# Performance work log

Measured on AMD Instinct MI355X. Metric: run time of the kernel, lower is better.

Reference implementation:

```python
import jax, jax.numpy as jnp
import numpy as np


def _conv(x, w):
    # SpykeTorch snn.Convolution: plain conv2d, no bias, no padding (VALID)
    return jax.lax.conv_general_dilated(
        x, w, window_strides=(1, 1), padding='VALID',
        dimension_numbers=('NCHW', 'OIHW', 'NCHW'))


def _pad2(x, p=2):
    # sf.pad(input, pad=(2,2,2,2), value=0): zero-pad last two (spatial) dims
    return jnp.pad(x, ((0, 0), (0, 0), (p, p), (p, p)))


def _fire(pot, thr):
    # sf.fire: thresholded[pot <= thr] = 0 ; spk = thresholded.sign()
    thresholded = jnp.where(pot > thr, pot, jnp.zeros((), pot.dtype))
    spk = (pot > thr).astype(pot.dtype)
    return spk, thresholded


def _pool(x, k, s):
    # sf.pooling: max_pool2d, floor mode (== VALID reduce_window)
    return jax.lax.reduce_window(
        x, -jnp.inf, jax.lax.max,
        window_dimensions=(1, 1, k, k),
        window_strides=(1, 1, s, s),
        padding='VALID')


def setup_inputs() -> dict:
    key = jax.random.key(0)
    kx, k1, k2, k3 = jax.random.split(key, 4)
    # (T, C, H, W): T timesteps act as batch in SpykeTorch
    x = jax.random.uniform(kx, (20, 6, 160, 160), dtype=jnp.float32)

    def xavier_normal(k, shape):
        fan_in = shape[1] * shape[2] * shape[3]
        fan_out = shape[0] * shape[2] * shape[3]
        std = float(np.sqrt(2.0 / (fan_in + fan_out)))
        return jax.random.normal(k, shape, dtype=jnp.float32) * std

    w1 = xavier_normal(k1, (30, 6, 4, 4))
    w2 = xavier_normal(k2, (250, 30, 3, 3))
    w3 = xavier_normal(k3, (200, 250, 3, 3))
    return {'x': x, 'w1': w1, 'w2': w2, 'w3': w3, 'layer_idx': 3}


def reference(x, w1, w2, w3, layer_idx):
    # Eval-mode forward path of deepSNN up to `layer_idx` (tensor-returning branches)
    CONV1_T, CONV2_T, CONV3_T = 1.0, 1.0, 25.0
    inp = _pad2(x.astype(jnp.float32))          # (T,6,164,164)
    pot = _conv(inp, w1)                        # (T,30,161,161)
    spk, pot = _fire(pot, CONV1_T)
    if layer_idx == 1:
        return spk, pot
    pot = _conv(_pad2(_pool(spk, 2, 2)), w2)    # (T,250,82,82)
    spk, pot = _fire(pot, CONV2_T)
    if layer_idx == 2:
        return spk, pot
    pot = _conv(_pad2(_pool(spk, 3, 3)), w3)    # (T,200,29,29)
    spk, pot = _fire(pot, CONV3_T)
    return spk, pot
```

## Files before the change

kernel.cpp:

```cpp
#include <hip/hip_runtime.h>


#define OUT_HALF 3364000
#define MASK_PLANE 128000
#define T_FLOATS 168200

typedef float v2f __attribute__((ext_vector_type(2)));

__global__ __launch_bounds__(256, 4) void k_conv1(const float* __restrict__ x,
                                                  const float* __restrict__ w1,
                                                  const float* __restrict__ w2,
                                                  float* __restrict__ w2t,
                                                  unsigned int* __restrict__ mask1,
                                                  unsigned int* __restrict__ flags2) {
    if (blockIdx.x >= 1500) {
        int tb = blockIdx.x - 1500;
        int tid = threadIdx.x;
        if (tb == 0)
            for (int i = tid; i < 540; i += 256) flags2[i] = 0u;
        int idx = tb * 256 + tid;
        if (idx < 67500) {
            int oc = idx / 270, ck = idx % 270;
            w2t[ck * 250 + oc] = w2[idx];
        }
        return;
    }

    __shared__ float in_lds[6 * 35 * 40];

    int b = blockIdx.x;
    int h = b % 3;     b /= 3;
    int colt = b % 5;  b /= 5;
    int rowt = b % 5;  b /= 5;
    int t = b;
    int ph0 = rowt * 16, pw0 = colt * 16;
    int i0 = 2 * ph0, j0 = 2 * pw0;
    int tid = threadIdx.x;

    for (int idx = tid; idx < 2100; idx += 256) {
        int v4 = idx % 10;
        int row = idx / 10;
        int c = row / 35, rr = row % 35;
        int gr = i0 + rr - 2;
        int gc0 = j0 - 4 + 4 * v4;
        float4 v; v.x = 0.f; v.y = 0.f; v.z = 0.f; v.w = 0.f;
        if ((unsigned)gr < 160u && (unsigned)gc0 < 160u)
            v = *(const float4*)&x[((t * 6 + c) * 160 + gr) * 160 + gc0];
        float* dst = &in_lds[row * 40];
        int m = 2 * v4;
        dst[m]      = v.x;
        dst[m + 20] = v.y;
        dst[m + 1]  = v.z;
        dst[m + 21] = v.w;
    }
    __syncthreads();

    int pw_l = tid & 15, ph_l = tid >> 4;
    int rb = 2 * ph_l;

    v2f acc01[10], acc23[10];
#pragma unroll
    for (int o = 0; o < 10; ++o) {
        acc01[o] = (v2f)(0.f);
        acc23[o] = (v2f)(0.f);
    }

    const float4* wq = (const float4*)w1 + h * 10 * 24;

#pragma unroll 1
    for (int c = 0; c < 6; ++c) {
        const float* pl = &in_lds[(c * 35 + rb) * 40 + pw_l];
        float q[5][5];
#pragma unroll
        for (int r = 0; r < 5; ++r) {
            const float* pr = pl + r * 40;
            q[r][0] = pr[1];  q[r][1] = pr[21]; q[r][2] = pr[2];
            q[r][3] = pr[22]; q[r][4] = pr[3];
        }
        v2f p[5][4];
#pragma unroll
        for (int r = 0; r < 5; ++r)
#pragma unroll
            for (int k = 0; k < 4; ++k) {
                p[r][k].x = q[r][k];
                p[r][k].y = q[r][k + 1];
            }
#pragma unroll
        for (int o = 0; o < 10; ++o) {
            const float4* wp = wq + o * 24 + c * 4;
#pragma unroll
            for (int kh = 0; kh < 4; ++kh) {
                float4 wv = wp[kh];
                v2f w0 = {wv.x, wv.x}, w1v = {wv.y, wv.y};
                v2f w2v = {wv.z, wv.z}, w3v = {wv.w, wv.w};
                acc01[o] += p[kh][0] * w0;   acc23[o] += p[kh + 1][0] * w0;
                acc01[o] += p[kh][1] * w1v;  acc23[o] += p[kh + 1][1] * w1v;
                acc01[o] += p[kh][2] * w2v;  acc23[o] += p[kh + 1][2] * w2v;
                acc01[o] += p[kh][3] * w3v;  acc23[o] += p[kh + 1][3] * w3v;
            }
        }
    }

    unsigned int msk = 0;
#pragma unroll
    for (int o = 0; o < 10; ++o) {
        bool s = acc01[o].x > 1.f || acc01[o].y > 1.f ||
                 acc23[o].x > 1.f || acc23[o].y > 1.f;
        if (s) msk |= 1u << o;
    }
    mask1[h * MASK_PLANE + (t * 80 + ph0 + ph_l) * 80 + pw0 + pw_l] = msk;
}

__global__ __launch_bounds__(256) void k_conv2(const unsigned int* __restrict__ mask1,
                                               const float* __restrict__ w2t,
                                               unsigned long long* __restrict__ pool2m,
                                               unsigned int* __restrict__ flags2) {
    __shared__ unsigned int m_lds[5 * 84];
    __shared__ int f2;

    int b = blockIdx.x;
    int ninth = b % 9;  b /= 9;
    int ph = b % 27;
    int t = b / 27;
    int tid = threadIdx.x;
    int ocl = tid & 63, wv = tid >> 6;
    int r0 = 3 * ph - 2;
    int pwA = ninth * 3;

    if (tid == 0) f2 = 0;
    for (int idx = tid; idx < 420; idx += 256) {
        int r = idx / 84, col = idx % 84;
        int gr = r0 + r, gc = col - 2;
        unsigned int v = 0;
        if ((unsigned)gr < 80u && (unsigned)gc < 80u) {
            int i2 = (t * 80 + gr) * 80 + gc;
            v = mask1[i2] | (mask1[MASK_PLANE + i2] << 10) |
                (mask1[2 * MASK_PLANE + i2] << 20);
        }
        m_lds[idx] = v;
    }
    __syncthreads();

    int oc = wv * 64 + ocl;
    const float* wb = w2t + oc;
    bool valid = oc < 250;
    unsigned long long* prow = pool2m + ((t * 27 + ph) * 27) * 4 + wv;

    {
        int c0A = 3 * pwA, c0B = c0A + 3;
        unsigned int qA[25], qB[25];
#pragma unroll
        for (int dr = 0; dr < 5; ++dr)
#pragma unroll
            for (int ds = 0; ds < 5; ++ds) {
                qA[dr * 5 + ds] = m_lds[dr * 84 + c0A + ds];
                qB[dr * 5 + ds] = m_lds[dr * 84 + c0B + ds];
            }

        float accA[3][3], accB[3][3];
#pragma unroll
        for (int i = 0; i < 3; ++i)
#pragma unroll
            for (int j = 0; j < 3; ++j) { accA[i][j] = 0.f; accB[i][j] = 0.f; }

#pragma unroll
        for (int dr = 0; dr < 5; ++dr) {
#pragma unroll
            for (int ds = 0; ds < 5; ++ds) {
                unsigned int mA = qA[dr * 5 + ds];
                unsigned int mB = qB[dr * 5 + ds];
                while (mA | mB) {
                    bool hA = mA != 0, hB = mB != 0;
                    int cA = __builtin_ctz(mA | 0x40000000u);
                    int cB = __builtin_ctz(mB | 0x40000000u);
                    mA &= mA - 1;
                    mB &= mB - 1;
                    const float* pA = wb + cA * 2250;
                    const float* pB = wb + cB * 2250;
                    float vA[3][3], vB[3][3];
#pragma unroll
                    for (int i = 0; i < 3; ++i) {
                        if (dr - i < 0 || dr - i > 2) continue;
#pragma unroll
                        for (int j = 0; j < 3; ++j) {
                            if (ds - j < 0 || ds - j > 2) continue;
                            int off = ((dr - i) * 3 + (ds - j)) * 250;
                            vA[i][j] = pA[off];
                            vB[i][j] = pB[off];
                        }
                    }
#pragma unroll
                    for (int i = 0; i < 3; ++i) {
                        if (dr - i < 0 || dr - i > 2) continue;
#pragma unroll
                        for (int j = 0; j < 3; ++j) {
                            if (ds - j < 0 || ds - j > 2) continue;
                            accA[i][j] += hA ? vA[i][j] : 0.f;
                            accB[i][j] += hB ? vB[i][j] : 0.f;
                        }
                    }
                }
            }
        }

        bool sA = false, sB = false;
#pragma unroll
        for (int i = 0; i < 3; ++i)
#pragma unroll
            for (int j = 0; j < 3; ++j) {
                sA = sA || (accA[i][j] > 1.f);
                sB = sB || (accB[i][j] > 1.f);
            }
        unsigned long long bA = __ballot(sA && valid);
        unsigned long long bB = __ballot(sB && valid);
        if (ocl == 0) {
            prow[pwA * 4] = bA;
            prow[(pwA + 1) * 4] = bB;
        }
        if (bA | bB) f2 = 1;
    }

    {
        int pw = pwA + 2;
        int c0 = 3 * pw;
        unsigned int q[25];
#pragma unroll
        for (int dr = 0; dr < 5; ++dr)
#pragma unroll
            for (int ds = 0; ds < 5; ++ds)
                q[dr * 5 + ds] = m_lds[dr * 84 + c0 + ds];

        float acc[3][3];
#pragma unroll
        for (int i = 0; i < 3; ++i)
#pragma unroll
            for (int j = 0; j < 3; ++j) acc[i][j] = 0.f;

#pragma unroll
        for (int dr = 0; dr < 5; ++dr) {
#pragma unroll
            for (int ds = 0; ds < 5; ++ds) {
                unsigned int m = q[dr * 5 + ds];
                while (m) {
                    int c1 = __builtin_ctz(m); m &= m - 1;
                    bool has2 = (m != 0);
                    int c2 = c1;
                    if (has2) { c2 = __builtin_ctz(m); m &= m - 1; }
                    const float* p1 = wb + c1 * 2250;
                    const float* p2 = wb + c2 * 2250;
                    float v1[3][3], v2[3][3];
#pragma unroll
                    for (int i = 0; i < 3; ++i) {
                        if (dr - i < 0 || dr - i > 2) continue;
#pragma unroll
                        for (int j = 0; j < 3; ++j) {
                            if (ds - j < 0 || ds - j > 2) continue;
                            int off = ((dr - i) * 3 + (ds - j)) * 250;
                            v1[i][j] = p1[off];
                            v2[i][j] = p2[off];
                        }
                    }
#pragma unroll
                    for (int i = 0; i < 3; ++i) {
                        if (dr - i < 0 || dr - i > 2) continue;
#pragma unroll
                        for (int j = 0; j < 3; ++j) {
                            if (ds - j < 0 || ds - j > 2) continue;
                            acc[i][j] += v1[i][j];
                            acc[i][j] += has2 ? v2[i][j] : 0.f;
                        }
                    }
                }
            }
        }

        bool s = false;
#pragma unroll
        for (int i = 0; i < 3; ++i)
#pragma unroll
            for (int j = 0; j < 3; ++j) s = s || (acc[i][j] > 1.f);

        unsigned long long blt = __ballot(s && valid);
        if (ocl == 0) prow[pw * 4] = blt;
        if (blt) f2 = 1;
    }

    __syncthreads();
    if (tid == 0 && f2) flags2[t * 27 + ph] = 1u;
}

__global__ __launch_bounds__(320) void k_conv3(const unsigned long long* __restrict__ pool2m,
                                               const float* __restrict__ w3,
                                               float* __restrict__ out,
                                               const unsigned int* __restrict__ flags2) {
    __shared__ float w_lds[25 * 9 * 40];
    __shared__ float in_lds[25 * 4 * 34];

    int b = blockIdx.x;
    int rb = b % 15;  b /= 15;
    int ocg = b % 5;  b /= 5;
    int t = b;
    int oc0 = ocg * 40;
    int r0 = 2 * rb;
    int tid = threadIdx.x;
    int ocl = tid % 40, ct = tid / 40;

    {
        unsigned int fT = 0;
        const unsigned int* fp = flags2 + t * 27;
#pragma unroll
        for (int r = 0; r < 27; ++r) fT |= fp[r];
        if (fT == 0) {
            float4 z; z.x = 0.f; z.y = 0.f; z.z = 0.f; z.w = 0.f;
            float4* o0 = (float4*)(out + (size_t)t * T_FLOATS);
            float4* o1 = (float4*)(out + OUT_HALF + (size_t)t * T_FLOATS);
            int s = ocg * 15 + rb;
            int lo = s * 561;
            int hi = lo + 561; if (hi > 42050) hi = 42050;
            for (int i = lo + tid; i < hi; i += 320) {
                o0[i] = z;
                o1[i] = z;
            }
            return;
        }
    }

    {
        unsigned int f = 0;
        int rlo = r0 - 2; if (rlo < 0) rlo = 0;
        int rhi = r0 + 1; if (rhi > 26) rhi = 26;
        for (int r = rlo; r <= rhi; ++r) f |= flags2[t * 27 + r];
        if (f == 0) {
            int nrows = (r0 + 1 < 29) ? 2 : 1;
            int stride = 29 * nrows;
            int cnt = 40 * stride;
            for (int idx = tid; idx < cnt; idx += 320) {
                int o = idx / stride, rem = idx % stride;
                size_t base = (size_t)((t * 200 + oc0 + o) * 29 + r0) * 29 + rem;
                out[base] = 0.f;
                out[OUT_HALF + base] = 0.f;
            }
            return;
        }
    }

    float acc[2][4];
#pragma unroll
    for (int i = 0; i < 2; ++i)
#pragma unroll
        for (int j = 0; j < 4; ++j) acc[i][j] = 0.f;

    for (int chn = 0; chn < 10; ++chn) {
        int cc0 = chn * 25;
        for (int idx = tid; idx < 25 * 9 * 40; idx += 320) {
            int o = idx % 40, ck = idx / 40;
            int ckg = cc0 * 9 + ck;
            w_lds[idx] = w3[(size_t)(oc0 + o) * 2250 + ckg];
        }
        for (int idx = tid; idx < 25 * 4 * 34; idx += 320) {
            int col = idx % 34;
            int rem = idx / 34;
            int r = rem & 3, cl = rem >> 2;
            int gr = r0 + r - 2, gc = col - 2;
            float v = 0.f;
            if ((unsigned)gr < 27u && (unsigned)gc < 27u) {
                int c = cc0 + cl;
                unsigned long long wbits =
                    pool2m[((t * 27 + gr) * 27 + gc) * 4 + (c >> 6)];
                v = (float)((wbits >> (c & 63)) & 1ull);
            }
            in_lds[idx] = v;
        }
        __syncthreads();

        for (int cl = 0; cl < 25; ++cl) {
            float in[4][6];
#pragma unroll
            for (int r = 0; r < 4; ++r)
#pragma unroll
                for (int j = 0; j < 6; ++j)
                    in[r][j] = in_lds[(cl * 4 + r) * 34 + ct * 4 + j];
            const float* wp = &w_lds[cl * 360 + ocl];
#pragma unroll
            for (int k = 0; k < 9; ++k) {
                float w = wp[k * 40];
                int kh = k / 3, kw = k % 3;
#pragma unroll
                for (int i = 0; i < 2; ++i)
#pragma unroll
                    for (int j = 0; j < 4; ++j)
                        acc[i][j] += in[i + kh][j + kw] * w;
            }
        }
        __syncthreads();
    }

    {
        int oc = oc0 + ocl;
#pragma unroll
        for (int i = 0; i < 2; ++i) {
            int r = r0 + i;
            if (r < 29) {
#pragma unroll
                for (int j = 0; j < 4; ++j) {
                    int col = ct * 4 + j;
                    if (col < 29) {
                        float pot = acc[i][j];
                        bool s = pot > 25.f;
                        size_t base = ((size_t)((t * 200 + oc) * 29 + r)) * 29 + col;
                        out[base] = s ? 1.f : 0.f;
                        out[OUT_HALF + base] = s ? pot : 0.f;
                    }
                }
            }
        }
    }
}

extern "C" void kernel_launch(void* const* d_in, const int* in_sizes, int n_in,
                              void* d_out, int out_size, void* d_ws, size_t ws_size,
                              hipStream_t stream) {
    const float* x  = (const float*)d_in[0];
    const float* w1 = (const float*)d_in[1];
    const float* w2 = (const float*)d_in[2];
    const float* w3 = (const float*)d_in[3];
    float* out = (float*)d_out;

    unsigned int* mask1 = (unsigned int*)d_ws;
    unsigned long long* pool2m = (unsigned long long*)((char*)d_ws + 1536000);
    float* w2t = (float*)((char*)d_ws + 2002560);
    unsigned int* flags2 = (unsigned int*)((char*)d_ws + 2277376);

    k_conv1<<<1764, 256, 0, stream>>>(x, w1, w2, w2t, mask1, flags2);
    k_conv2<<<20 * 27 * 9, 256, 0, stream>>>(mask1, w2t, pool2m, flags2);
    k_conv3<<<20 * 5 * 15, 320, 0, stream>>>(pool2m, w3, out, flags2);
}
```

Before: 142.4 us.

## Compute conv1 with bf16 MFMA on a pre-padded input buffer

Replaces the scalar FP32 conv1 kernel with a new kernel that treats the 4x4x6 convolution as a small GEMM using 32x32x16 bf16 MFMA instructions. Pooled spike masks are built with wave ballots. A new prep kernel zero-pads the input into a workspace buffer and also absorbs the w2 transpose and flag clearing that conv1 used to do. The intent is to move conv1 arithmetic onto matrix cores. It costs an extra kernel launch, a full write and read of the padded input, and bf16 rounding that can flip spikes whose potential lies near the threshold.

```diff
diff --git a/kernel.cpp b/kernel.cpp
--- a/kernel.cpp
+++ b/kernel.cpp
@@ -1,21 +1,36 @@
 #include <hip/hip_runtime.h>
+#include <hip/hip_bf16.h>
 
 
 #define OUT_HALF 3364000
 #define MASK_PLANE 128000
 #define T_FLOATS 168200
 
-typedef float v2f __attribute__((ext_vector_type(2)));
-
-__global__ __launch_bounds__(256, 4) void k_conv1(const float* __restrict__ x,
-                                                  const float* __restrict__ w1,
-                                                  const float* __restrict__ w2,
-                                                  float* __restrict__ w2t,
-                                                  unsigned int* __restrict__ mask1,
-                                                  unsigned int* __restrict__ flags2) {
-    if (blockIdx.x >= 1500) {
-        int tb = blockIdx.x - 1500;
-        int tid = threadIdx.x;
+typedef float f32x16 __attribute__((ext_vector_type(16)));
+typedef short bf8s __attribute__((ext_vector_type(8)));
+typedef float f32x4 __attribute__((ext_vector_type(4)));
+typedef f32x4 f32x4u __attribute__((aligned(4)));
+
+static __device__ __forceinline__ unsigned int pkbf(float a, float b) {
+    union { __hip_bfloat162 h; unsigned int u; } cv;
+    cv.h = __float22bfloat162_rn(make_float2(a, b));
+    return cv.u;
+}
+static __device__ __forceinline__ unsigned short bfbits(float a) {
+    union { __hip_bfloat16 h; unsigned short u; } cv;
+    cv.h = __float2bfloat16(a);
+    return cv.u;
+}
+
+__global__ __launch_bounds__(256) void k_prep(const float* __restrict__ x,
+                                              const float* __restrict__ w2,
+                                              float* __restrict__ xpad,
+                                              float* __restrict__ w2t,
+                                              unsigned int* __restrict__ flags2) {
+    int bidx = blockIdx.x;
+    int tid = threadIdx.x;
+    if (bidx >= 1576) {
+        int tb = bidx - 1576;
         if (tb == 0)
             for (int i = tid; i < 540; i += 256) flags2[i] = 0u;
         int idx = tb * 256 + tid;
@@ -25,90 +40,85 @@
         }
         return;
     }
-
-    __shared__ float in_lds[6 * 35 * 40];
-
+    for (int e = bidx * 256 + tid; e < 3227520; e += 403456) {
+        int tc = e / 26896;
+        int rem = e - tc * 26896;
+        int r = rem / 164, col = rem - r * 164;
+        int sr = r - 2, sc = col - 2;
+        float v = 0.f;
+        if ((unsigned)sr < 160u && (unsigned)sc < 160u)
+            v = x[(tc * 160 + sr) * 160 + sc];
+        xpad[e] = v;
+    }
+}
+
+__global__ __launch_bounds__(256) void k_conv1m(const float* __restrict__ xpad,
+                                                const float* __restrict__ w1,
+                                                unsigned int* __restrict__ mask1) {
+    __shared__ unsigned short B_lds[6 * 64 * 8];
+
+    int tid = threadIdx.x;
+#pragma unroll
+    for (int n = 0; n < 12; ++n) {
+        int q = n * 256 + tid;
+        int i = q & 7, ll = (q >> 3) & 63, ks = q >> 9;
+        int oc = ll & 31;
+        int kg = ks * 16 + ((ll >> 5) << 3) + i;
+        float w = (oc < 30) ? w1[oc * 96 + kg] : 0.f;
+        B_lds[q] = bfbits(w);
+    }
+    __syncthreads();
+
+    int l = tid & 63, wv = tid >> 6;
     int b = blockIdx.x;
-    int h = b % 3;     b /= 3;
-    int colt = b % 5;  b /= 5;
-    int rowt = b % 5;  b /= 5;
-    int t = b;
-    int ph0 = rowt * 16, pw0 = colt * 16;
-    int i0 = 2 * ph0, j0 = 2 * pw0;
-    int tid = threadIdx.x;
-
-    for (int idx = tid; idx < 2100; idx += 256) {
-        int v4 = idx % 10;
-        int row = idx / 10;
-        int c = row / 35, rr = row % 35;
-        int gr = i0 + rr - 2;
-        int gc0 = j0 - 4 + 4 * v4;
-        float4 v; v.x = 0.f; v.y = 0.f; v.z = 0.f; v.w = 0.f;
-        if ((unsigned)gr < 160u && (unsigned)gc0 < 160u)
-            v = *(const float4*)&x[((t * 6 + c) * 160 + gr) * 160 + gc0];
-        float* dst = &in_lds[row * 40];
-        int m = 2 * v4;
-        dst[m]      = v.x;
-        dst[m + 20] = v.y;
-        dst[m + 1]  = v.z;
-        dst[m + 21] = v.w;
-    }
-    __syncthreads();
-
-    int pw_l = tid & 15, ph_l = tid >> 4;
-    int rb = 2 * ph_l;
-
-    v2f acc01[10], acc23[10];
-#pragma unroll
-    for (int o = 0; o < 10; ++o) {
-        acc01[o] = (v2f)(0.f);
-        acc23[o] = (v2f)(0.f);
-    }
-
-    const float4* wq = (const float4*)w1 + h * 10 * 24;
-
-#pragma unroll 1
-    for (int c = 0; c < 6; ++c) {
-        const float* pl = &in_lds[(c * 35 + rb) * 40 + pw_l];
-        float q[5][5];
-#pragma unroll
-        for (int r = 0; r < 5; ++r) {
-            const float* pr = pl + r * 40;
-            q[r][0] = pr[1];  q[r][1] = pr[21]; q[r][2] = pr[2];
-            q[r][3] = pr[22]; q[r][4] = pr[3];
-        }
-        v2f p[5][4];
-#pragma unroll
-        for (int r = 0; r < 5; ++r)
-#pragma unroll
-            for (int k = 0; k < 4; ++k) {
-                p[r][k].x = q[r][k];
-                p[r][k].y = q[r][k + 1];
-            }
-#pragma unroll
-        for (int o = 0; o < 10; ++o) {
-            const float4* wp = wq + o * 24 + c * 4;
-#pragma unroll
-            for (int kh = 0; kh < 4; ++kh) {
-                float4 wv = wp[kh];
-                v2f w0 = {wv.x, wv.x}, w1v = {wv.y, wv.y};
-                v2f w2v = {wv.z, wv.z}, w3v = {wv.w, wv.w};
-                acc01[o] += p[kh][0] * w0;   acc23[o] += p[kh + 1][0] * w0;
-                acc01[o] += p[kh][1] * w1v;  acc23[o] += p[kh + 1][1] * w1v;
-                acc01[o] += p[kh][2] * w2v;  acc23[o] += p[kh + 1][2] * w2v;
-                acc01[o] += p[kh][3] * w3v;  acc23[o] += p[kh + 1][3] * w3v;
-            }
-        }
-    }
-
-    unsigned int msk = 0;
-#pragma unroll
-    for (int o = 0; o < 10; ++o) {
-        bool s = acc01[o].x > 1.f || acc01[o].y > 1.f ||
-                 acc23[o].x > 1.f || acc23[o].y > 1.f;
-        if (s) msk |= 1u << o;
-    }
-    mask1[h * MASK_PLANE + (t * 80 + ph0 + ph_l) * 80 + pw0 + pw_l] = msk;
+    int t = b / 100;
+    int u = (b % 100) * 4 + wv;
+    int pr = u / 5, jblk = u % 5;
+    int m = l & 31, hi = l >> 5;
+    int j = jblk * 32 + m;
+
+    bf8s bq[6];
+#pragma unroll
+    for (int ks = 0; ks < 6; ++ks)
+        bq[ks] = *(const bf8s*)&B_lds[(ks * 64 + l) * 8];
+
+    f32x16 acc0 = (f32x16)(0.0f);
+    f32x16 acc1 = (f32x16)(0.0f);
+    int r0 = 2 * pr + 2 * hi;
+
+#pragma unroll
+    for (int ks = 0; ks < 6; ++ks) {
+        const float* base = xpad + ((t * 6 + ks) * 164 + r0) * 164 + j;
+        f32x4 v0 = *(const f32x4u*)(base);
+        f32x4 v1 = *(const f32x4u*)(base + 164);
+        f32x4 v2 = *(const f32x4u*)(base + 328);
+        union { bf8s s; unsigned int u4[4]; } a0, a1;
+        a0.u4[0] = pkbf(v0.x, v0.y);
+        a0.u4[1] = pkbf(v0.z, v0.w);
+        a0.u4[2] = pkbf(v1.x, v1.y);
+        a0.u4[3] = pkbf(v1.z, v1.w);
+        a1.u4[0] = a0.u4[2];
+        a1.u4[1] = a0.u4[3];
+        a1.u4[2] = pkbf(v2.x, v2.y);
+        a1.u4[3] = pkbf(v2.z, v2.w);
+        acc0 = __builtin_amdgcn_mfma_f32_32x32x16_bf16(a0.s, bq[ks], acc0, 0, 0, 0);
+        acc1 = __builtin_amdgcn_mfma_f32_32x32x16_bf16(a1.s, bq[ks], acc1, 0, 0, 0);
+    }
+
+    unsigned int mbase = (unsigned int)((t * 80 + pr) * 80 + jblk * 16);
+#pragma unroll
+    for (int a = 0; a < 8; ++a) {
+        bool s = acc0[2 * a] > 1.f || acc0[2 * a + 1] > 1.f ||
+                 acc1[2 * a] > 1.f || acc1[2 * a + 1] > 1.f;
+        unsigned long long bal = __ballot(s);
+        if (l < 6) {
+            int h = l >> 1;
+            unsigned int word = (l & 1) ? (unsigned int)(bal >> 32)
+                                        : (unsigned int)bal;
+            int pc = (a & 1) + ((a >> 1) << 2) + ((l & 1) << 1);
+            mask1[h * MASK_PLANE + mbase + pc] = (word >> (10 * h)) & 0x3FFu;
+        }
+    }
 }
 
 __global__ __launch_bounds__(256) void k_conv2(const unsigned int* __restrict__ mask1,
@@ -430,8 +440,10 @@
     unsigned long long* pool2m = (unsigned long long*)((char*)d_ws + 1536000);
     float* w2t = (float*)((char*)d_ws + 2002560);
     unsigned int* flags2 = (unsigned int*)((char*)d_ws + 2277376);
-
-    k_conv1<<<1764, 256, 0, stream>>>(x, w1, w2, w2t, mask1, flags2);
+    float* xpad = (float*)((char*)d_ws + 4194304);
+
+    k_prep<<<1840, 256, 0, stream>>>(x, w2, xpad, w2t, flags2);
+    k_conv1m<<<2000, 256, 0, stream>>>(xpad, w1, mask1);
     k_conv2<<<20 * 27 * 9, 256, 0, stream>>>(mask1, w2t, pool2m, flags2);
     k_conv3<<<20 * 5 * 15, 320, 0, stream>>>(pool2m, w3, out, flags2);
 }
```

Result: faster. 127.1 us (-10.8%).
